# Kernel optimization log

Hardware: AMD Instinct MI355X
Metric: run time of the kernel (lower is better)

Reference implementation:

```python
import jax, jax.numpy as jnp
import numpy as np

NUM_NODES = 100000
NUM_EDGES = 400000
F_IN = 16          # num_node_features
F_EDGE = 8         # num_edge_features
EMB = 16           # emb_size
NUM_GRAPHS = 256


def setup_inputs() -> dict:
    key = jax.random.key(0)
    ks = jax.random.split(key, 12)
    x = jax.random.normal(ks[0], (NUM_NODES, F_IN), dtype=jnp.float32)
    edge_index = jax.random.randint(ks[1], (2, NUM_EDGES), 0, NUM_NODES, dtype=jnp.int32)
    edge_attr = jax.random.normal(ks[2], (NUM_EDGES, F_EDGE), dtype=jnp.float32)
    batch = jnp.sort(jax.random.randint(ks[3], (NUM_NODES,), 0, NUM_GRAPHS, dtype=jnp.int32))
    s = 0.1
    # edge-network MLP: Linear(F_EDGE -> F_IN*EMB) + ReLU (torch Linear convention: W[out,in])
    nn1_w = jax.random.normal(ks[4], (F_IN * EMB, F_EDGE), dtype=jnp.float32) * s
    nn1_b = jax.random.normal(ks[5], (F_IN * EMB,), dtype=jnp.float32) * s
    # NNConv root weight (bias=False Linear) + separate bias
    root_w = jax.random.normal(ks[6], (EMB, F_IN), dtype=jnp.float32) * s
    conv_b = jax.random.normal(ks[7], (EMB,), dtype=jnp.float32) * s
    lin1_w = jax.random.normal(ks[8], (EMB, 2 * EMB), dtype=jnp.float32) * s
    lin1_b = jax.random.normal(ks[9], (EMB,), dtype=jnp.float32) * s
    lin2_w = jax.random.normal(ks[10], (1, EMB), dtype=jnp.float32) * s
    lin2_b = jax.random.normal(ks[11], (1,), dtype=jnp.float32) * s
    return {"x": x, "edge_index": edge_index, "edge_attr": edge_attr, "batch": batch,
            "nn1_w": nn1_w, "nn1_b": nn1_b, "root_w": root_w, "conv_b": conv_b,
            "lin1_w": lin1_w, "lin1_b": lin1_b, "lin2_w": lin2_w, "lin2_b": lin2_b}


def reference(x, edge_index, edge_attr, batch, nn1_w, nn1_b, root_w, conv_b,
              lin1_w, lin1_b, lin2_w, lin2_b):
    N = x.shape[0]
    src, dst = edge_index[0], edge_index[1]  # PyG: message flows src(j) -> dst(i)
    # edge network -> per-edge weight matrices [E, F_IN, EMB]
    w = jax.nn.relu(edge_attr @ nn1_w.T + nn1_b).reshape(-1, F_IN, EMB)
    # gather source features, per-edge matmul
    msg = jnp.einsum('ei,eio->eo', x[src], w)  # [E, EMB]
    # scatter-mean into target nodes
    sums = jax.ops.segment_sum(msg, dst, num_segments=N)
    cnt = jax.ops.segment_sum(jnp.ones((msg.shape[0],), msg.dtype), dst, num_segments=N)
    agg = sums / jnp.maximum(cnt, 1.0)[:, None]
    # NNConv: root transform + aggregated messages + bias, then outer ReLU
    h = jax.nn.relu(agg + x @ root_w.T + conv_b)  # [N, EMB]
    # global max pool and global mean pool per graph
    gmax = jax.ops.segment_max(h, batch, num_segments=NUM_GRAPHS)
    gsum = jax.ops.segment_sum(h, batch, num_segments=NUM_GRAPHS)
    gcnt = jax.ops.segment_sum(jnp.ones((N,), h.dtype), batch, num_segments=NUM_GRAPHS)
    gmean = gsum / jnp.maximum(gcnt, 1.0)[:, None]
    pooled = jnp.concatenate([gmax, gmean], axis=1)  # [G, 2*EMB]
    h2 = jax.nn.relu(pooled @ lin1_w.T + lin1_b)
    out = h2 @ lin2_w.T + lin2_b  # [G, 1]
    return out
```

## Files before the change

### kernel.cpp

```cpp
#include <hip/hip_runtime.h>

#define NUM_NODES 100000
#define NUM_EDGES 400000
#define F_IN 16
#define F_EDGE 8
#define EMB 16
#define NUM_GRAPHS 256

#define EDGE_TILES 5
#define EDGE_BLOCKS (NUM_EDGES / (32 * EDGE_TILES))

#define NPB 128
#define NODE_BLOCKS ((NUM_NODES + NPB - 1) / NPB)


__global__ __launch_bounds__(256) void edge_kernel(
    const float* __restrict__ x, const int* __restrict__ ei,
    const float* __restrict__ ea, const float* __restrict__ nn1_w,
    const float* __restrict__ nn1_b, float* __restrict__ sums,
    float* __restrict__ cnt)
{
    __shared__ float wtp[256 * 12];
    __shared__ float btp[16 * 20];

    const int tid = threadIdx.x;
    const int eL  = tid >> 4;
    const int o   = tid & 15;

    #pragma unroll
    for (int t = tid; t < F_IN * EMB * F_EDGE; t += 256)
        wtp[(t >> 3) * 12 + (t & 7)] = nn1_w[t];
    btp[(tid & 15) * 20 + (tid >> 4)] = nn1_b[tid];
    __syncthreads();

    float br[F_IN];
    #pragma unroll
    for (int r = 0; r < 4; r++) {
        const float4 b4 = *(const float4*)&btp[o * 20 + 4 * r];
        br[4 * r + 0] = b4.x; br[4 * r + 1] = b4.y;
        br[4 * r + 2] = b4.z; br[4 * r + 3] = b4.w;
    }

    for (int t = 0; t < EDGE_TILES; t++) {
        const int e0 = (blockIdx.x * EDGE_TILES + t) * 32;
        const int eA = e0 + eL;
        const int eB = e0 + 16 + eL;

        const int srcA = ei[eA];
        const int srcB = ei[eB];
        const int dstA = ei[NUM_EDGES + eA];
        const int dstB = ei[NUM_EDGES + eB];

        const float4 a00 = *(const float4*)&ea[eA * 8];
        const float4 a01 = *(const float4*)&ea[eA * 8 + 4];
        const float4 a10 = *(const float4*)&ea[eB * 8];
        const float4 a11 = *(const float4*)&ea[eB * 8 + 4];

        float xr0[F_IN], xr1[F_IN];
        #pragma unroll
        for (int r = 0; r < 4; r++) {
            const float4 v0 = *(const float4*)&x[srcA * 16 + 4 * r];
            const float4 v1 = *(const float4*)&x[srcB * 16 + 4 * r];
            xr0[4 * r + 0] = v0.x; xr0[4 * r + 1] = v0.y;
            xr0[4 * r + 2] = v0.z; xr0[4 * r + 3] = v0.w;
            xr1[4 * r + 0] = v1.x; xr1[4 * r + 1] = v1.y;
            xr1[4 * r + 2] = v1.z; xr1[4 * r + 3] = v1.w;
        }

        float acc0 = 0.f, acc1 = 0.f;
        #pragma unroll
        for (int i = 0; i < F_IN; i++) {
            const float* wr = &wtp[(i * 16 + o) * 12];
            const float4 w0 = *(const float4*)wr;
            const float4 w1 = *(const float4*)(wr + 4);
            float u = br[i];
            u = fmaf(a00.x, w0.x, u); u = fmaf(a00.y, w0.y, u);
            u = fmaf(a00.z, w0.z, u); u = fmaf(a00.w, w0.w, u);
            u = fmaf(a01.x, w1.x, u); u = fmaf(a01.y, w1.y, u);
            u = fmaf(a01.z, w1.z, u); u = fmaf(a01.w, w1.w, u);
            acc0 = fmaf(xr0[i], fmaxf(u, 0.f), acc0);
            float v = br[i];
            v = fmaf(a10.x, w0.x, v); v = fmaf(a10.y, w0.y, v);
            v = fmaf(a10.z, w0.z, v); v = fmaf(a10.w, w0.w, v);
            v = fmaf(a11.x, w1.x, v); v = fmaf(a11.y, w1.y, v);
            v = fmaf(a11.z, w1.z, v); v = fmaf(a11.w, w1.w, v);
            acc1 = fmaf(xr1[i], fmaxf(v, 0.f), acc1);
        }

        atomicAdd(&sums[dstA * 16 + o], acc0);
        atomicAdd(&sums[dstB * 16 + o], acc1);
        if (o == 0) {
            atomicAdd(&cnt[dstA], 1.f);
            atomicAdd(&cnt[dstB], 1.f);
        }
    }
}

__global__ __launch_bounds__(256) void node_kernel(
    const float* __restrict__ x, const int* __restrict__ batch,
    const float* __restrict__ root_w, const float* __restrict__ conv_b,
    const float* __restrict__ sums, const float* __restrict__ cnt,
    unsigned int* __restrict__ gmax, float* __restrict__ gsum,
    float* __restrict__ gcnt)
{
    __shared__ float rwT[256];
    __shared__ float xsh[256];
    __shared__ float ssh[256];
    __shared__ float csh[16];
    __shared__ int   bsh[16];
    __shared__ float hsh[256];

    const int tid = threadIdx.x;
    const int j   = tid >> 4;
    const int o   = tid & 15;
    const int n0  = blockIdx.x * NPB;

    rwT[(tid & 15) * 16 + (tid >> 4)] = root_w[tid];
    const float cb = conv_b[o];

    int   curg = batch[n0];
    float am = 0.f, asum = 0.f, ac = 0.f;

    for (int s0 = 0; s0 < NPB; s0 += 16) {
        const int base = n0 + s0;
        const int idx  = base * 16 + tid;
        const bool v   = (idx < NUM_NODES * 16);
        const float xv = v ? x[idx]    : 0.f;
        const float sv = v ? sums[idx] : 0.f;
        float cv = 1.f; int bv = -1;
        if (tid < 16) {
            const int n = base + tid;
            if (n < NUM_NODES) { cv = cnt[n]; bv = batch[n]; }
        }
        __syncthreads();
        xsh[tid] = xv; ssh[tid] = sv;
        if (tid < 16) { csh[tid] = cv; bsh[tid] = bv; }
        __syncthreads();

        float a = cb + ssh[j * 16 + o] / fmaxf(csh[j], 1.f);
        #pragma unroll
        for (int i = 0; i < F_IN; i++)
            a = fmaf(xsh[j * 16 + i], rwT[i * 16 + o], a);
        hsh[tid] = fmaxf(a, 0.f);
        __syncthreads();

        if (tid < 16) {
            #pragma unroll 1
            for (int jj = 0; jj < 16; jj++) {
                const int g = bsh[jj];
                if (g < 0) break;
                if (g != curg) {
                    atomicMax(&gmax[curg * 16 + o], __float_as_uint(am));
                    atomicAdd(&gsum[curg * 16 + o], asum);
                    if (o == 0) atomicAdd(&gcnt[curg], ac);
                    am = 0.f; asum = 0.f; ac = 0.f; curg = g;
                }
                const float h = hsh[jj * 16 + o];
                am = fmaxf(am, h); asum += h; ac += 1.f;
            }
        }
    }

    if (tid < 16) {
        atomicMax(&gmax[curg * 16 + o], __float_as_uint(am));
        atomicAdd(&gsum[curg * 16 + o], asum);
        if (o == 0) atomicAdd(&gcnt[curg], ac);
    }
}

__global__ __launch_bounds__(256) void head_kernel(
    const unsigned int* __restrict__ gmax, const float* __restrict__ gsum,
    const float* __restrict__ gcnt,
    const float* __restrict__ lin1_w, const float* __restrict__ lin1_b,
    const float* __restrict__ lin2_w, const float* __restrict__ lin2_b,
    float* __restrict__ out)
{
    const int g = threadIdx.x;

    float pooled[2 * EMB];
    #pragma unroll
    for (int o = 0; o < EMB; o++) pooled[o] = __uint_as_float(gmax[g * 16 + o]);
    const float c = fmaxf(gcnt[g], 1.f);
    #pragma unroll
    for (int o = 0; o < EMB; o++) pooled[EMB + o] = gsum[g * 16 + o] / c;

    float acc = lin2_b[0];
    #pragma unroll
    for (int k = 0; k < EMB; k++) {
        float a = lin1_b[k];
        #pragma unroll
        for (int cc = 0; cc < 2 * EMB; cc++)
            a = fmaf(pooled[cc], lin1_w[k * 32 + cc], a);
        acc = fmaf(fmaxf(a, 0.f), lin2_w[k], acc);
    }
    out[g] = acc;
}

extern "C" void kernel_launch(void* const* d_in, const int* in_sizes, int n_in,
                              void* d_out, int out_size, void* d_ws, size_t ws_size,
                              hipStream_t stream) {
    const float* x      = (const float*)d_in[0];
    const int*   ei     = (const int*)d_in[1];
    const float* ea     = (const float*)d_in[2];
    const int*   batch  = (const int*)d_in[3];
    const float* nn1_w  = (const float*)d_in[4];
    const float* nn1_b  = (const float*)d_in[5];
    const float* root_w = (const float*)d_in[6];
    const float* conv_b = (const float*)d_in[7];
    const float* lin1_w = (const float*)d_in[8];
    const float* lin1_b = (const float*)d_in[9];
    const float* lin2_w = (const float*)d_in[10];
    const float* lin2_b = (const float*)d_in[11];
    float* out = (float*)d_out;

    float*        sums = (float*)d_ws;
    float*        cnt  = sums + (size_t)NUM_NODES * EMB;
    unsigned int* gmax = (unsigned int*)(cnt + NUM_NODES);
    float*        gsum = (float*)(gmax + NUM_GRAPHS * EMB);
    float*        gcnt = gsum + NUM_GRAPHS * EMB;

    const size_t zero_bytes = sizeof(float) *
        ((size_t)NUM_NODES * EMB + NUM_NODES + 2 * NUM_GRAPHS * EMB + NUM_GRAPHS);
    hipMemsetAsync(d_ws, 0, zero_bytes, stream);

    edge_kernel<<<EDGE_BLOCKS, 256, 0, stream>>>(x, ei, ea, nn1_w, nn1_b, sums, cnt);
    node_kernel<<<NODE_BLOCKS, 256, 0, stream>>>(
        x, batch, root_w, conv_b, sums, cnt, gmax, gsum, gcnt);
    head_kernel<<<1, 256, 0, stream>>>(gmax, gsum, gcnt,
                                       lin1_w, lin1_b, lin2_w, lin2_b, out);
}
```

Measured before the change: 165.6 us.

## Register-resident edge weights, split input dim across lanes, prefetched grid-stride edge loop

The edge kernel now keeps the edge-network weights in registers instead of LDS, with each pair of 16-lane groups splitting the 16 input features in half and combining partial sums via a cross-lane shuffle. It becomes a persistent grid-stride loop over 8-edge tiles, software-prefetching the next tile's indices, attributes and source features while computing the current one. The hipMemsetAsync is replaced by a custom zeroing kernel. This trades LDS traffic and per-block weight reloads for higher register pressure, and halves atomics per lane group but processes fewer edges per thread per iteration.

```diff
diff --git a/kernel.cpp b/kernel.cpp
--- a/kernel.cpp
+++ b/kernel.cpp
@@ -7,92 +7,86 @@
 #define EMB 16
 #define NUM_GRAPHS 256
 
-#define EDGE_TILES 5
-#define EDGE_BLOCKS (NUM_EDGES / (32 * EDGE_TILES))
+#define NT (NUM_EDGES / 8)
+#define EDGE_GRID 2048
 
 #define NPB 128
 #define NODE_BLOCKS ((NUM_NODES + NPB - 1) / NPB)
 
-
-__global__ __launch_bounds__(256) void edge_kernel(
+#define WS_ZERO_FLOATS (NUM_NODES * EMB + NUM_NODES + 2 * NUM_GRAPHS * EMB + NUM_GRAPHS)
+
+__global__ __launch_bounds__(256) void zero_kernel(float4* __restrict__ ws)
+{
+    const int n4 = WS_ZERO_FLOATS / 4;
+    const int stride = gridDim.x * 256;
+    for (int i = blockIdx.x * 256 + threadIdx.x; i < n4; i += stride)
+        ws[i] = make_float4(0.f, 0.f, 0.f, 0.f);
+}
+
+__global__ __launch_bounds__(256, 3) void edge_kernel(
     const float* __restrict__ x, const int* __restrict__ ei,
     const float* __restrict__ ea, const float* __restrict__ nn1_w,
     const float* __restrict__ nn1_b, float* __restrict__ sums,
     float* __restrict__ cnt)
 {
-    __shared__ float wtp[256 * 12];
-    __shared__ float btp[16 * 20];
-
     const int tid = threadIdx.x;
-    const int eL  = tid >> 4;
     const int o   = tid & 15;
-
-    #pragma unroll
-    for (int t = tid; t < F_IN * EMB * F_EDGE; t += 256)
-        wtp[(t >> 3) * 12 + (t & 7)] = nn1_w[t];
-    btp[(tid & 15) * 20 + (tid >> 4)] = nn1_b[tid];
-    __syncthreads();
-
-    float br[F_IN];
-    #pragma unroll
-    for (int r = 0; r < 4; r++) {
-        const float4 b4 = *(const float4*)&btp[o * 20 + 4 * r];
-        br[4 * r + 0] = b4.x; br[4 * r + 1] = b4.y;
-        br[4 * r + 2] = b4.z; br[4 * r + 3] = b4.w;
-    }
-
-    for (int t = 0; t < EDGE_TILES; t++) {
-        const int e0 = (blockIdx.x * EDGE_TILES + t) * 32;
-        const int eA = e0 + eL;
-        const int eB = e0 + 16 + eL;
-
-        const int srcA = ei[eA];
-        const int srcB = ei[eB];
-        const int dstA = ei[NUM_EDGES + eA];
-        const int dstB = ei[NUM_EDGES + eB];
-
-        const float4 a00 = *(const float4*)&ea[eA * 8];
-        const float4 a01 = *(const float4*)&ea[eA * 8 + 4];
-        const float4 a10 = *(const float4*)&ea[eB * 8];
-        const float4 a11 = *(const float4*)&ea[eB * 8 + 4];
-
-        float xr0[F_IN], xr1[F_IN];
+    const int ih  = (tid >> 4) & 1;
+    const int eL  = tid >> 5;
+
+    float4 w0[8], w1[8];
+    float  br[8];
+    #pragma unroll
+    for (int ii = 0; ii < 8; ii++) {
+        const int r = (ih * 8 + ii) * 16 + o;
+        w0[ii] = *(const float4*)&nn1_w[r * 8];
+        w1[ii] = *(const float4*)&nn1_w[r * 8 + 4];
+        br[ii] = nn1_b[r];
+    }
+
+    int t = blockIdx.x;
+    int e   = t * 8 + eL;
+    int src = ei[e];
+    int dst = ei[NUM_EDGES + e];
+    float4 a0 = *(const float4*)&ea[e * 8];
+    float4 a1 = *(const float4*)&ea[e * 8 + 4];
+    float4 x0 = *(const float4*)&x[src * 16 + ih * 8];
+    float4 x1 = *(const float4*)&x[src * 16 + ih * 8 + 4];
+
+    while (true) {
+        const int tn = t + EDGE_GRID;
+        const bool more = (tn < NT);
+        int srcn = 0, dstn = 0;
+        float4 na0, na1, nx0, nx1;
+        if (more) {
+            const int en = tn * 8 + eL;
+            srcn = ei[en];
+            dstn = ei[NUM_EDGES + en];
+            na0 = *(const float4*)&ea[en * 8];
+            na1 = *(const float4*)&ea[en * 8 + 4];
+            nx0 = *(const float4*)&x[srcn * 16 + ih * 8];
+            nx1 = *(const float4*)&x[srcn * 16 + ih * 8 + 4];
+        }
+
+        const float xr[8] = {x0.x, x0.y, x0.z, x0.w, x1.x, x1.y, x1.z, x1.w};
+        float acc = 0.f;
         #pragma unroll
-        for (int r = 0; r < 4; r++) {
-            const float4 v0 = *(const float4*)&x[srcA * 16 + 4 * r];
-            const float4 v1 = *(const float4*)&x[srcB * 16 + 4 * r];
-            xr0[4 * r + 0] = v0.x; xr0[4 * r + 1] = v0.y;
-            xr0[4 * r + 2] = v0.z; xr0[4 * r + 3] = v0.w;
-            xr1[4 * r + 0] = v1.x; xr1[4 * r + 1] = v1.y;
-            xr1[4 * r + 2] = v1.z; xr1[4 * r + 3] = v1.w;
-        }
-
-        float acc0 = 0.f, acc1 = 0.f;
-        #pragma unroll
-        for (int i = 0; i < F_IN; i++) {
-            const float* wr = &wtp[(i * 16 + o) * 12];
-            const float4 w0 = *(const float4*)wr;
-            const float4 w1 = *(const float4*)(wr + 4);
-            float u = br[i];
-            u = fmaf(a00.x, w0.x, u); u = fmaf(a00.y, w0.y, u);
-            u = fmaf(a00.z, w0.z, u); u = fmaf(a00.w, w0.w, u);
-            u = fmaf(a01.x, w1.x, u); u = fmaf(a01.y, w1.y, u);
-            u = fmaf(a01.z, w1.z, u); u = fmaf(a01.w, w1.w, u);
-            acc0 = fmaf(xr0[i], fmaxf(u, 0.f), acc0);
-            float v = br[i];
-            v = fmaf(a10.x, w0.x, v); v = fmaf(a10.y, w0.y, v);
-            v = fmaf(a10.z, w0.z, v); v = fmaf(a10.w, w0.w, v);
-            v = fmaf(a11.x, w1.x, v); v = fmaf(a11.y, w1.y, v);
-            v = fmaf(a11.z, w1.z, v); v = fmaf(a11.w, w1.w, v);
-            acc1 = fmaf(xr1[i], fmaxf(v, 0.f), acc1);
-        }
-
-        atomicAdd(&sums[dstA * 16 + o], acc0);
-        atomicAdd(&sums[dstB * 16 + o], acc1);
-        if (o == 0) {
-            atomicAdd(&cnt[dstA], 1.f);
-            atomicAdd(&cnt[dstB], 1.f);
-        }
+        for (int ii = 0; ii < 8; ii++) {
+            float u = br[ii];
+            u = fmaf(a0.x, w0[ii].x, u); u = fmaf(a0.y, w0[ii].y, u);
+            u = fmaf(a0.z, w0[ii].z, u); u = fmaf(a0.w, w0[ii].w, u);
+            u = fmaf(a1.x, w1[ii].x, u); u = fmaf(a1.y, w1[ii].y, u);
+            u = fmaf(a1.z, w1[ii].z, u); u = fmaf(a1.w, w1[ii].w, u);
+            acc = fmaf(xr[ii], fmaxf(u, 0.f), acc);
+        }
+        acc += __shfl_xor(acc, 16);
+
+        if (ih == 0)         atomicAdd(&sums[dst * 16 + o], acc);
+        if ((tid & 31) == 0) atomicAdd(&cnt[dst], 1.f);
+
+        if (!more) break;
+        t = tn; src = srcn; dst = dstn;
+        a0 = na0; a1 = na1; x0 = nx0; x1 = nx1;
     }
 }
 
@@ -219,11 +213,8 @@
     float*        gsum = (float*)(gmax + NUM_GRAPHS * EMB);
     float*        gcnt = gsum + NUM_GRAPHS * EMB;
 
-    const size_t zero_bytes = sizeof(float) *
-        ((size_t)NUM_NODES * EMB + NUM_NODES + 2 * NUM_GRAPHS * EMB + NUM_GRAPHS);
-    hipMemsetAsync(d_ws, 0, zero_bytes, stream);
-
-    edge_kernel<<<EDGE_BLOCKS, 256, 0, stream>>>(x, ei, ea, nn1_w, nn1_b, sums, cnt);
+    zero_kernel<<<1024, 256, 0, stream>>>((float4*)d_ws);
+    edge_kernel<<<EDGE_GRID, 256, 0, stream>>>(x, ei, ea, nn1_w, nn1_b, sums, cnt);
     node_kernel<<<NODE_BLOCKS, 256, 0, stream>>>(
         x, batch, root_w, conv_b, sums, cnt, gmax, gsum, gcnt);
     head_kernel<<<1, 256, 0, stream>>>(gmax, gsum, gcnt,
```

Result: slower. 171.7 us (+3.7%).
